# Kernel tuning notes

Hardware: AMD Instinct MI355X
Metric: run time of the kernel (lower is better)

The kernel has to match this reference:

```python
import jax, jax.numpy as jnp
from jax import lax
import numpy as np

NUM_CAPS = 4
CAP_DIM = 8
NUM_CLASSES = 10
CLASS_DIM = 16


def squash(x):
    # x: [..., D]; scale = |x|^2/(1+|x|^2)/sqrt(|x|^2+1e-8)
    sq = jnp.sum(x * x, axis=-1, keepdims=True)
    return sq / (1.0 + sq) / jnp.sqrt(sq + 1e-8) * x


def primary_caps(x, w, b):
    # x: [B,C,H,W], w: [32,C,3,3] -> caps [B, H*W*NUM_CAPS, CAP_DIM]
    out = lax.conv_general_dilated(
        x, w, window_strides=(1, 1), padding=[(1, 1), (1, 1)],
        dimension_numbers=('NCHW', 'OIHW', 'NCHW')) + b[None, :, None, None]
    B, C, H, W = out.shape
    out = out.reshape(B, NUM_CAPS, CAP_DIM, H * W)
    out = out.transpose(0, 3, 1, 2).reshape(B, H * W * NUM_CAPS, CAP_DIM)
    return squash(out)


def setup_inputs() -> dict:
    key = jax.random.key(0)
    ks = jax.random.split(key, 7)
    B, H, Wd = 64, 32, 32
    hsi_c, sar_c = 144, 4
    N = 2 * H * Wd * NUM_CAPS  # 8192
    return {
        'x_hsi': jax.random.normal(ks[0], (B, hsi_c, H, Wd), jnp.float32),
        'x_sar': jax.random.normal(ks[1], (B, sar_c, H, Wd), jnp.float32),
        'wh': jax.random.normal(ks[2], (NUM_CAPS * CAP_DIM, hsi_c, 3, 3), jnp.float32) * 0.05,
        'bh': jax.random.normal(ks[3], (NUM_CAPS * CAP_DIM,), jnp.float32) * 0.05,
        'ws': jax.random.normal(ks[4], (NUM_CAPS * CAP_DIM, sar_c, 3, 3), jnp.float32) * 0.05,
        'bs': jax.random.normal(ks[5], (NUM_CAPS * CAP_DIM,), jnp.float32) * 0.05,
        'W': jax.random.normal(ks[6], (N, NUM_CLASSES, CLASS_DIM, CAP_DIM), jnp.float32),
    }


def reference(x_hsi, x_sar, wh, bh, ws, bs, W):
    caps_h = primary_caps(x_hsi, wh, bh)
    caps_s = primary_caps(x_sar, ws, bs)
    caps = jnp.concatenate([caps_h, caps_s], axis=1)  # [B, N, D]
    N = caps.shape[1]
    # routing_iters=1 with b=0 => c = 1/N uniform; s = sum_n c*u_hat = mean_n u_hat
    # u_hat[b,n,c,j] = sum_d W[n,c,j,d] * caps[b,n,d] (fused, never materialized)
    s = jnp.einsum('bnd,ncjd->bcj', caps, W) / N  # [B, num_classes, class_dim]
    v = squash(s)
    logits = jnp.sqrt(jnp.sum(v * v, axis=-1))  # [B, num_classes]
    return logits
```

## Files before the change

### kernel.cpp

```cpp
#include <hip/hip_runtime.h>
#include <hip/hip_bf16.h>


#define B_SZ 64
#define HW 32

typedef __attribute__((ext_vector_type(8))) short bf16x8s;
typedef __attribute__((ext_vector_type(4))) float f32x4;

__device__ inline short f2bf(float f) {
    __hip_bfloat16 h = __float2bfloat16(f);
    return *reinterpret_cast<short*>(&h);
}

__global__ __launch_bounds__(256) void prep_w_kernel(const float* __restrict__ wh,
                                                     short* __restrict__ wtb) {
    int idx = blockIdx.x * 256 + threadIdx.x;
    int tap = idx / 5120;
    int rest = idx - tap * 5120;
    int oc = rest / 160;
    int cin = rest - oc * 160;
    short v = 0;
    if (cin < 144) v = f2bf(wh[(oc * 144 + cin) * 9 + tap]);
    wtb[idx] = v;
}

__global__ __launch_bounds__(256) void prep_x_kernel(const float* __restrict__ xin,
                                                     short* __restrict__ xb) {
    __shared__ short tile[160 * 33];
    int t = threadIdx.x;
    int b = blockIdx.x >> 5;
    int y = blockIdx.x & 31;
    for (int idx = t; idx < 512; idx += 256) {
        int x = idx & 31, cin = 144 + (idx >> 5);
        tile[cin * 33 + x] = 0;
    }
    for (int base = 0; base < 144; base += 8) {
        int cin = base + (t >> 5), x = t & 31;
        float v = xin[(((size_t)b * 144 + cin) * 32 + y) * 32 + x];
        tile[cin * 33 + x] = f2bf(v);
    }
    __syncthreads();
    unsigned* dst = (unsigned*)(xb + ((size_t)(b * 32 + y) * 32) * 160);
    for (int idx = t; idx < 2560; idx += 256) {
        int x = idx / 80;
        int cinp = idx - x * 80;
        unsigned lo = (unsigned short)tile[(2 * cinp) * 33 + x];
        unsigned hi = (unsigned short)tile[(2 * cinp + 1) * 33 + x];
        dst[idx] = lo | (hi << 16);
    }
}

__global__ void transpose_w_kernel(const float* __restrict__ w, float* __restrict__ wt,
                                   int cin_total) {
    int idx = blockIdx.x * blockDim.x + threadIdx.x;
    int total = 32 * cin_total * 9;
    if (idx >= total) return;
    int oc = idx & 31;
    int rest = idx >> 5;
    int tap = rest % 9;
    int cin = rest / 9;
    wt[idx] = w[(oc * cin_total + cin) * 9 + tap];
}

__global__ __launch_bounds__(256) void conv_mfma_kernel(
        const short* __restrict__ xb, const short* __restrict__ wtb,
        const float* __restrict__ bias, short* __restrict__ capsb) {
    __shared__ float ctile[64][34];
    int t = threadIdx.x;
    int l = t & 63;
    int wv = t >> 6;
    int mhalf = wv >> 1;
    int nt = wv & 1;
    int l15 = l & 15, lhi = l >> 4;
    int b = blockIdx.x >> 4;
    int y0 = (blockIdx.x & 15) << 1;
    int y = y0 + mhalf;
    int kofs = lhi * 8;

    const short* xbb = xb + (size_t)b * 1024 * 160;

    f32x4 acc0 = {0.f, 0.f, 0.f, 0.f};
    f32x4 acc1 = {0.f, 0.f, 0.f, 0.f};
    const bf16x8s zfrag = {0, 0, 0, 0, 0, 0, 0, 0};

    #pragma unroll
    for (int tap = 0; tap < 9; ++tap) {
        int dy = tap / 3, dx = tap % 3;
        int iy = y + dy - 1;
        bool rowok = (unsigned)iy < 32u;
        int iyc = rowok ? iy : 0;
        int ix0 = l15 + dx - 1;
        int ix1 = 16 + l15 + dx - 1;
        bool ok0 = rowok && ((unsigned)ix0 < 32u);
        bool ok1 = rowok && ((unsigned)ix1 < 32u);
        int ix0c = min(max(ix0, 0), 31);
        int ix1c = min(max(ix1, 0), 31);
        const short* xa0 = xbb + ((size_t)(iyc * 32 + ix0c)) * 160 + kofs;
        const short* xa1 = xbb + ((size_t)(iyc * 32 + ix1c)) * 160 + kofs;
        const short* wa = wtb + ((size_t)tap * 32 + nt * 16 + l15) * 160 + kofs;
        #pragma unroll
        for (int kc = 0; kc < 5; ++kc) {
            bf16x8s bfrag = *(const bf16x8s*)(wa + kc * 32);
            bf16x8s a0 = *(const bf16x8s*)(xa0 + kc * 32);
            bf16x8s a1 = *(const bf16x8s*)(xa1 + kc * 32);
            a0 = ok0 ? a0 : zfrag;
            a1 = ok1 ? a1 : zfrag;
            acc0 = __builtin_amdgcn_mfma_f32_16x16x32_bf16(a0, bfrag, acc0, 0, 0, 0);
            acc1 = __builtin_amdgcn_mfma_f32_16x16x32_bf16(a1, bfrag, acc1, 0, 0, 0);
        }
    }

    #pragma unroll
    for (int r = 0; r < 4; ++r) {
        ctile[mhalf * 32 + lhi * 4 + r][nt * 16 + l15] = acc0[r];
        ctile[mhalf * 32 + 16 + lhi * 4 + r][nt * 16 + l15] = acc1[r];
    }
    __syncthreads();

    int p = t >> 2;
    int cap = t & 3;
    float s[8];
    float sq = 0.0f;
    #pragma unroll
    for (int d = 0; d < 8; ++d) {
        s[d] = ctile[p][cap * 8 + d] + bias[cap * 8 + d];
        sq += s[d] * s[d];
    }
    float scale = sq / ((1.0f + sq) * sqrtf(sq + 1e-8f));
    int pix = (y0 + (p >> 5)) * 32 + (p & 31);
    int n = pix * 4 + cap;
    bf16x8s o;
    #pragma unroll
    for (int d = 0; d < 8; ++d) o[d] = f2bf(s[d] * scale);
    *(bf16x8s*)(capsb + ((size_t)b * 8192 + n) * 8) = o;
}

__global__ __launch_bounds__(256) void conv_caps_sar_kernel(
        const float* __restrict__ xin, const float* __restrict__ wt,
        const float* __restrict__ bias, short* __restrict__ capsb, int n_base) {
    constexpr int CIN = 4;
    __shared__ float red[4][32][64];
    int t = threadIdx.x;
    int wave = __builtin_amdgcn_readfirstlane(t >> 6);
    int lane = t & 63;
    int x = lane & 31;
    int yy = lane >> 5;
    int bidx = blockIdx.x;
    int b = bidx >> 4;
    int y = ((bidx & 15) << 1) + yy;

    const float* xb_ = xin + (size_t)b * CIN * (HW * HW);

    float acc[32];
    #pragma unroll
    for (int oc = 0; oc < 32; ++oc) acc[oc] = 0.0f;

    {
        int cin = wave;
        const float* xc = xb_ + (size_t)cin * (HW * HW);
        const float* wc = wt + (size_t)cin * 288;
        #pragma unroll
        for (int ky = 0; ky < 3; ++ky) {
            int iy = y + ky - 1;
            bool rowok = (iy >= 0) && (iy < HW);
            const float* xrow = xc + iy * HW;
            float v0 = (rowok && x > 0)      ? xrow[x - 1] : 0.0f;
            float v1 = rowok                 ? xrow[x]     : 0.0f;
            float v2 = (rowok && x < HW - 1) ? xrow[x + 1] : 0.0f;
            const float* wk = wc + ky * 96;
            #pragma unroll
            for (int oc = 0; oc < 32; ++oc) {
                acc[oc] += v0 * wk[oc] + v1 * wk[32 + oc] + v2 * wk[64 + oc];
            }
        }
    }

    #pragma unroll
    for (int oc = 0; oc < 32; ++oc) red[wave][oc][lane] = acc[oc];
    __syncthreads();

    int cap = t >> 6;
    int p = t & 63;
    float s[8];
    float sq = 0.0f;
    #pragma unroll
    for (int d = 0; d < 8; ++d) {
        int oc = cap * 8 + d;
        s[d] = bias[oc] + red[0][oc][p] + red[1][oc][p] + red[2][oc][p] + red[3][oc][p];
        sq += s[d] * s[d];
    }
    float scale = sq / ((1.0f + sq) * sqrtf(sq + 1e-8f));
    int pix = (((bidx & 15) << 1) + (p >> 5)) * HW + (p & 31);
    int n = n_base + pix * 4 + cap;
    bf16x8s o;
    #pragma unroll
    for (int d = 0; d < 8; ++d) o[d] = f2bf(s[d] * scale);
    *(bf16x8s*)(capsb + ((size_t)b * 8192 + n) * 8) = o;
}

__global__ __launch_bounds__(256) void routing_mfma_kernel(
        const short* __restrict__ capsb, const float* __restrict__ W,
        float* __restrict__ partials) {
    __shared__ float red[4][64][18];
    int t = threadIdx.x;
    int l = t & 63;
    int wv = t >> 6;
    int l15 = l & 15, lhi = l >> 4;
    int kc = blockIdx.x;
    int ntile = blockIdx.y;
    int cj = ntile * 16 + l15;

    f32x4 acc[4] = {{0.f,0.f,0.f,0.f},{0.f,0.f,0.f,0.f},{0.f,0.f,0.f,0.f},{0.f,0.f,0.f,0.f}};

    int kk0 = kc * 32 + wv * 8;
    for (int ks = 0; ks < 8; ++ks) {
        int n = (kk0 + ks) * 4 + lhi;
        const float* wp = W + ((size_t)n * 160 + cj) * 8;
        float4 w0 = *(const float4*)wp;
        float4 w1 = *(const float4*)(wp + 4);
        union { short s[8]; bf16x8s v; } bu;
        bu.s[0] = f2bf(w0.x); bu.s[1] = f2bf(w0.y);
        bu.s[2] = f2bf(w0.z); bu.s[3] = f2bf(w0.w);
        bu.s[4] = f2bf(w1.x); bu.s[5] = f2bf(w1.y);
        bu.s[6] = f2bf(w1.z); bu.s[7] = f2bf(w1.w);
        const short* ap = capsb + (size_t)n * 8;
        #pragma unroll
        for (int mt = 0; mt < 4; ++mt) {
            int b = mt * 16 + l15;
            bf16x8s afrag = *(const bf16x8s*)(ap + (size_t)b * 8192 * 8);
            acc[mt] = __builtin_amdgcn_mfma_f32_16x16x32_bf16(afrag, bu.v, acc[mt], 0, 0, 0);
        }
    }

    #pragma unroll
    for (int mt = 0; mt < 4; ++mt) {
        #pragma unroll
        for (int r = 0; r < 4; ++r) {
            red[wv][mt * 16 + lhi * 4 + r][l15] = acc[mt][r];
        }
    }
    __syncthreads();

    for (int idx = t; idx < 1024; idx += 256) {
        int b = idx >> 4, cjl = idx & 15;
        float sum = red[0][b][cjl] + red[1][b][cjl] + red[2][b][cjl] + red[3][b][cjl];
        partials[(((size_t)kc * 10 + ntile) * 64 + b) * 16 + cjl] = sum;
    }
}

__global__ __launch_bounds__(256) void finalize_kernel(
        const float* __restrict__ partials, float* __restrict__ out) {
    __shared__ float s_sh[160];
    int t = threadIdx.x;
    int b = blockIdx.x;
    if (t < 160) {
        int nt = t >> 4, cjl = t & 15;
        float s = 0.0f;
        #pragma unroll 8
        for (int kc = 0; kc < 64; ++kc)
            s += partials[(((size_t)kc * 10 + nt) * 64 + b) * 16 + cjl];
        s_sh[t] = s * (1.0f / 8192.0f);
    }
    __syncthreads();
    if (t < 10) {
        float sq = 0.0f;
        #pragma unroll
        for (int j = 0; j < 16; ++j) {
            float v = s_sh[t * 16 + j];
            sq += v * v;
        }
        float scale = sq / ((1.0f + sq) * sqrtf(sq + 1e-8f));
        out[b * 10 + t] = sqrtf(sq) * scale;
    }
}

extern "C" void kernel_launch(void* const* d_in, const int* in_sizes, int n_in,
                              void* d_out, int out_size, void* d_ws, size_t ws_size,
                              hipStream_t stream) {
    const float* x_hsi = (const float*)d_in[0];
    const float* x_sar = (const float*)d_in[1];
    const float* wh    = (const float*)d_in[2];
    const float* bh    = (const float*)d_in[3];
    const float* wsar  = (const float*)d_in[4];
    const float* bs    = (const float*)d_in[5];
    const float* W     = (const float*)d_in[6];
    float* out = (float*)d_out;

    char* ws = (char*)d_ws;
    short* wtb     = (short*)(ws + 0);
    float* wt_s    = (float*)(ws + 92672);
    short* xb      = (short*)(ws + 102400);
    short* capsb   = (short*)(ws + 21073920);
    float* partials = (float*)(ws + 29462528);

    prep_w_kernel<<<180, 256, 0, stream>>>(wh, wtb);
    prep_x_kernel<<<2048, 256, 0, stream>>>(x_hsi, xb);
    transpose_w_kernel<<<5, 256, 0, stream>>>(wsar, wt_s, 4);

    conv_mfma_kernel<<<1024, 256, 0, stream>>>(xb, wtb, bh, capsb);
    conv_caps_sar_kernel<<<1024, 256, 0, stream>>>(x_sar, wt_s, bs, capsb, 4096);

    routing_mfma_kernel<<<dim3(64, 10), 256, 0, stream>>>(capsb, W, partials);

    finalize_kernel<<<64, 256, 0, stream>>>(partials, out);
}
```

Baseline: 84.16 us.

## Fuse input conversion and both convolutions into one kernel, transpose caps layout

Drops the separate bf16 input-conversion and SAR weight transpose kernels. A single conv kernel now stages fp32 HSI rows into shared memory as bf16, computing four output rows per block with 2x2 MFMA tiles, while extra blocks compute the SAR conv directly. The caps buffer layout changes to [n][batch][8] so the routing kernel reads contiguous fragments, and routing uses twice as many K-split blocks. The intent is to remove the 20MB intermediate bf16 tensor round-trip and launch overhead. The SAR path is one block per image with serial scalar work, which may leave a long tail.

```diff
diff --git a/kernel.cpp b/kernel.cpp
--- a/kernel.cpp
+++ b/kernel.cpp
@@ -1,9 +1,6 @@
 #include <hip/hip_runtime.h>
 #include <hip/hip_bf16.h>
 
-
-#define B_SZ 64
-#define HW 32
 
 typedef __attribute__((ext_vector_type(8))) short bf16x8s;
 typedef __attribute__((ext_vector_type(4))) float f32x4;
@@ -16,6 +13,7 @@
 __global__ __launch_bounds__(256) void prep_w_kernel(const float* __restrict__ wh,
                                                      short* __restrict__ wtb) {
     int idx = blockIdx.x * 256 + threadIdx.x;
+    if (idx >= 46080) return;
     int tap = idx / 5120;
     int rest = idx - tap * 5120;
     int oc = rest / 160;
@@ -25,178 +23,155 @@
     wtb[idx] = v;
 }
 
-__global__ __launch_bounds__(256) void prep_x_kernel(const float* __restrict__ xin,
-                                                     short* __restrict__ xb) {
-    __shared__ short tile[160 * 33];
+__global__ __launch_bounds__(256) void conv_both_kernel(
+        const float* __restrict__ x_hsi, const short* __restrict__ wtb,
+        const float* __restrict__ bh,
+        const float* __restrict__ x_sar, const float* __restrict__ wsar,
+        const float* __restrict__ bs,
+        short* __restrict__ capsb) {
+    __shared__ union {
+        short xs[6][32][168];
+        float ct[128][33];
+    } sm;
     int t = threadIdx.x;
-    int b = blockIdx.x >> 5;
-    int y = blockIdx.x & 31;
-    for (int idx = t; idx < 512; idx += 256) {
-        int x = idx & 31, cin = 144 + (idx >> 5);
-        tile[cin * 33 + x] = 0;
-    }
-    for (int base = 0; base < 144; base += 8) {
-        int cin = base + (t >> 5), x = t & 31;
-        float v = xin[(((size_t)b * 144 + cin) * 32 + y) * 32 + x];
-        tile[cin * 33 + x] = f2bf(v);
-    }
-    __syncthreads();
-    unsigned* dst = (unsigned*)(xb + ((size_t)(b * 32 + y) * 32) * 160);
-    for (int idx = t; idx < 2560; idx += 256) {
-        int x = idx / 80;
-        int cinp = idx - x * 80;
-        unsigned lo = (unsigned short)tile[(2 * cinp) * 33 + x];
-        unsigned hi = (unsigned short)tile[(2 * cinp + 1) * 33 + x];
-        dst[idx] = lo | (hi << 16);
-    }
-}
-
-__global__ void transpose_w_kernel(const float* __restrict__ w, float* __restrict__ wt,
-                                   int cin_total) {
-    int idx = blockIdx.x * blockDim.x + threadIdx.x;
-    int total = 32 * cin_total * 9;
-    if (idx >= total) return;
-    int oc = idx & 31;
-    int rest = idx >> 5;
-    int tap = rest % 9;
-    int cin = rest / 9;
-    wt[idx] = w[(oc * cin_total + cin) * 9 + tap];
-}
-
-__global__ __launch_bounds__(256) void conv_mfma_kernel(
-        const short* __restrict__ xb, const short* __restrict__ wtb,
-        const float* __restrict__ bias, short* __restrict__ capsb) {
-    __shared__ float ctile[64][34];
-    int t = threadIdx.x;
-    int l = t & 63;
-    int wv = t >> 6;
-    int mhalf = wv >> 1;
-    int nt = wv & 1;
-    int l15 = l & 15, lhi = l >> 4;
-    int b = blockIdx.x >> 4;
-    int y0 = (blockIdx.x & 15) << 1;
-    int y = y0 + mhalf;
-    int kofs = lhi * 8;
-
-    const short* xbb = xb + (size_t)b * 1024 * 160;
-
-    f32x4 acc0 = {0.f, 0.f, 0.f, 0.f};
-    f32x4 acc1 = {0.f, 0.f, 0.f, 0.f};
-    const bf16x8s zfrag = {0, 0, 0, 0, 0, 0, 0, 0};
-
-    #pragma unroll
-    for (int tap = 0; tap < 9; ++tap) {
-        int dy = tap / 3, dx = tap % 3;
-        int iy = y + dy - 1;
-        bool rowok = (unsigned)iy < 32u;
-        int iyc = rowok ? iy : 0;
-        int ix0 = l15 + dx - 1;
-        int ix1 = 16 + l15 + dx - 1;
-        bool ok0 = rowok && ((unsigned)ix0 < 32u);
-        bool ok1 = rowok && ((unsigned)ix1 < 32u);
-        int ix0c = min(max(ix0, 0), 31);
-        int ix1c = min(max(ix1, 0), 31);
-        const short* xa0 = xbb + ((size_t)(iyc * 32 + ix0c)) * 160 + kofs;
-        const short* xa1 = xbb + ((size_t)(iyc * 32 + ix1c)) * 160 + kofs;
-        const short* wa = wtb + ((size_t)tap * 32 + nt * 16 + l15) * 160 + kofs;
-        #pragma unroll
-        for (int kc = 0; kc < 5; ++kc) {
-            bf16x8s bfrag = *(const bf16x8s*)(wa + kc * 32);
-            bf16x8s a0 = *(const bf16x8s*)(xa0 + kc * 32);
-            bf16x8s a1 = *(const bf16x8s*)(xa1 + kc * 32);
-            a0 = ok0 ? a0 : zfrag;
-            a1 = ok1 ? a1 : zfrag;
-            acc0 = __builtin_amdgcn_mfma_f32_16x16x32_bf16(a0, bfrag, acc0, 0, 0, 0);
-            acc1 = __builtin_amdgcn_mfma_f32_16x16x32_bf16(a1, bfrag, acc1, 0, 0, 0);
-        }
-    }
-
-    #pragma unroll
-    for (int r = 0; r < 4; ++r) {
-        ctile[mhalf * 32 + lhi * 4 + r][nt * 16 + l15] = acc0[r];
-        ctile[mhalf * 32 + 16 + lhi * 4 + r][nt * 16 + l15] = acc1[r];
-    }
-    __syncthreads();
-
-    int p = t >> 2;
-    int cap = t & 3;
-    float s[8];
-    float sq = 0.0f;
-    #pragma unroll
-    for (int d = 0; d < 8; ++d) {
-        s[d] = ctile[p][cap * 8 + d] + bias[cap * 8 + d];
-        sq += s[d] * s[d];
-    }
-    float scale = sq / ((1.0f + sq) * sqrtf(sq + 1e-8f));
-    int pix = (y0 + (p >> 5)) * 32 + (p & 31);
-    int n = pix * 4 + cap;
-    bf16x8s o;
-    #pragma unroll
-    for (int d = 0; d < 8; ++d) o[d] = f2bf(s[d] * scale);
-    *(bf16x8s*)(capsb + ((size_t)b * 8192 + n) * 8) = o;
-}
-
-__global__ __launch_bounds__(256) void conv_caps_sar_kernel(
-        const float* __restrict__ xin, const float* __restrict__ wt,
-        const float* __restrict__ bias, short* __restrict__ capsb, int n_base) {
-    constexpr int CIN = 4;
-    __shared__ float red[4][32][64];
-    int t = threadIdx.x;
-    int wave = __builtin_amdgcn_readfirstlane(t >> 6);
-    int lane = t & 63;
-    int x = lane & 31;
-    int yy = lane >> 5;
-    int bidx = blockIdx.x;
-    int b = bidx >> 4;
-    int y = ((bidx & 15) << 1) + yy;
-
-    const float* xb_ = xin + (size_t)b * CIN * (HW * HW);
-
-    float acc[32];
-    #pragma unroll
-    for (int oc = 0; oc < 32; ++oc) acc[oc] = 0.0f;
-
-    {
-        int cin = wave;
-        const float* xc = xb_ + (size_t)cin * (HW * HW);
-        const float* wc = wt + (size_t)cin * 288;
-        #pragma unroll
-        for (int ky = 0; ky < 3; ++ky) {
-            int iy = y + ky - 1;
-            bool rowok = (iy >= 0) && (iy < HW);
-            const float* xrow = xc + iy * HW;
-            float v0 = (rowok && x > 0)      ? xrow[x - 1] : 0.0f;
-            float v1 = rowok                 ? xrow[x]     : 0.0f;
-            float v2 = (rowok && x < HW - 1) ? xrow[x + 1] : 0.0f;
-            const float* wk = wc + ky * 96;
-            #pragma unroll
-            for (int oc = 0; oc < 32; ++oc) {
-                acc[oc] += v0 * wk[oc] + v1 * wk[32 + oc] + v2 * wk[64 + oc];
-            }
-        }
-    }
-
-    #pragma unroll
-    for (int oc = 0; oc < 32; ++oc) red[wave][oc][lane] = acc[oc];
-    __syncthreads();
-
-    int cap = t >> 6;
-    int p = t & 63;
-    float s[8];
-    float sq = 0.0f;
-    #pragma unroll
-    for (int d = 0; d < 8; ++d) {
-        int oc = cap * 8 + d;
-        s[d] = bias[oc] + red[0][oc][p] + red[1][oc][p] + red[2][oc][p] + red[3][oc][p];
-        sq += s[d] * s[d];
-    }
-    float scale = sq / ((1.0f + sq) * sqrtf(sq + 1e-8f));
-    int pix = (((bidx & 15) << 1) + (p >> 5)) * HW + (p & 31);
-    int n = n_base + pix * 4 + cap;
-    bf16x8s o;
-    #pragma unroll
-    for (int d = 0; d < 8; ++d) o[d] = f2bf(s[d] * scale);
-    *(bf16x8s*)(capsb + ((size_t)b * 8192 + n) * 8) = o;
+
+    if (blockIdx.x < 512) {
+        int b = blockIdx.x >> 3;
+        int y0 = (blockIdx.x & 7) << 2;
+
+        {
+            int x = t & 31;
+            int i0 = t >> 5;
+            const float* xb_ = x_hsi + (size_t)b * 144 * 1024;
+            for (int item = i0; item < 432; item += 8) {
+                int row = item / 72;
+                int cp = item - row * 72;
+                int iy = y0 - 1 + row;
+                unsigned u = 0;
+                if ((unsigned)iy < 32u) {
+                    float f0 = xb_[(size_t)(2 * cp) * 1024 + iy * 32 + x];
+                    float f1 = xb_[(size_t)(2 * cp + 1) * 1024 + iy * 32 + x];
+                    u = (unsigned)(unsigned short)f2bf(f0)
+                      | ((unsigned)(unsigned short)f2bf(f1) << 16);
+                }
+                *(unsigned*)&sm.xs[row][x][2 * cp] = u;
+            }
+            for (int item = i0; item < 48; item += 8) {
+                int row = item >> 3;
+                int c4 = item & 7;
+                *(unsigned*)&sm.xs[row][x][144 + 2 * c4] = 0;
+            }
+        }
+        __syncthreads();
+
+        int l = t & 63;
+        int wv = t >> 6;
+        int l15 = l & 15, lhi = l >> 4;
+        int kofs = lhi * 8;
+
+        f32x4 acc[2][2] = {{{0.f,0.f,0.f,0.f},{0.f,0.f,0.f,0.f}},
+                           {{0.f,0.f,0.f,0.f},{0.f,0.f,0.f,0.f}}};
+        const bf16x8s zf = {0,0,0,0,0,0,0,0};
+
+        #pragma unroll
+        for (int tap = 0; tap < 9; ++tap) {
+            int dy = tap / 3, dx = tap % 3;
+            int lrow = wv + dy;
+            int ix0 = l15 + dx - 1;
+            int ix1 = 16 + l15 + dx - 1;
+            bool ok0 = (unsigned)ix0 < 32u;
+            bool ok1 = (unsigned)ix1 < 32u;
+            int ix0c = ok0 ? ix0 : 0;
+            int ix1c = ok1 ? ix1 : 0;
+            const short* xa0 = &sm.xs[lrow][ix0c][kofs];
+            const short* xa1 = &sm.xs[lrow][ix1c][kofs];
+            const short* wa = wtb + ((size_t)tap * 32 + l15) * 160 + kofs;
+            #pragma unroll
+            for (int kc = 0; kc < 5; ++kc) {
+                bf16x8s a0 = *(const bf16x8s*)(xa0 + kc * 32);
+                bf16x8s a1 = *(const bf16x8s*)(xa1 + kc * 32);
+                a0 = ok0 ? a0 : zf;
+                a1 = ok1 ? a1 : zf;
+                bf16x8s b0 = *(const bf16x8s*)(wa + kc * 32);
+                bf16x8s b1 = *(const bf16x8s*)(wa + 16 * 160 + kc * 32);
+                acc[0][0] = __builtin_amdgcn_mfma_f32_16x16x32_bf16(a0, b0, acc[0][0], 0, 0, 0);
+                acc[0][1] = __builtin_amdgcn_mfma_f32_16x16x32_bf16(a0, b1, acc[0][1], 0, 0, 0);
+                acc[1][0] = __builtin_amdgcn_mfma_f32_16x16x32_bf16(a1, b0, acc[1][0], 0, 0, 0);
+                acc[1][1] = __builtin_amdgcn_mfma_f32_16x16x32_bf16(a1, b1, acc[1][1], 0, 0, 0);
+            }
+        }
+        __syncthreads();
+
+        #pragma unroll
+        for (int xh = 0; xh < 2; ++xh)
+            #pragma unroll
+            for (int nt = 0; nt < 2; ++nt)
+                #pragma unroll
+                for (int r = 0; r < 4; ++r)
+                    sm.ct[wv * 32 + xh * 16 + lhi * 4 + r][nt * 16 + l15] = acc[xh][nt][r];
+        __syncthreads();
+
+        #pragma unroll
+        for (int h = 0; h < 2; ++h) {
+            int q = t + h * 256;
+            int p = q >> 2;
+            int cap = q & 3;
+            float s[8];
+            float sq = 0.0f;
+            #pragma unroll
+            for (int d = 0; d < 8; ++d) {
+                s[d] = sm.ct[p][cap * 8 + d] + bh[cap * 8 + d];
+                sq += s[d] * s[d];
+            }
+            float scale = sq / ((1.0f + sq) * sqrtf(sq + 1e-8f));
+            int pix = (y0 + (p >> 5)) * 32 + (p & 31);
+            int n = pix * 4 + cap;
+            bf16x8s o;
+            #pragma unroll
+            for (int d = 0; d < 8; ++d) o[d] = f2bf(s[d] * scale);
+            *(bf16x8s*)(capsb + ((size_t)n * 64 + b) * 8) = o;
+        }
+    } else {
+        int b = blockIdx.x - 512;
+        const float* xb_ = x_sar + (size_t)b * 4 * 1024;
+        for (int i = 0; i < 4; ++i) {
+            int px = t + i * 256;
+            int y = px >> 5, x = px & 31;
+            float acc[32];
+            #pragma unroll
+            for (int oc = 0; oc < 32; ++oc) acc[oc] = bs[oc];
+            #pragma unroll
+            for (int tap = 0; tap < 9; ++tap) {
+                int dy = tap / 3, dx = tap % 3;
+                int iy = y + dy - 1, ix = x + dx - 1;
+                bool ok = ((unsigned)iy < 32u) && ((unsigned)ix < 32u);
+                int off = ok ? (iy * 32 + ix) : 0;
+                float v[4];
+                #pragma unroll
+                for (int ch = 0; ch < 4; ++ch) {
+                    float ld = xb_[(size_t)ch * 1024 + off];
+                    v[ch] = ok ? ld : 0.0f;
+                }
+                #pragma unroll
+                for (int oc = 0; oc < 32; ++oc)
+                    #pragma unroll
+                    for (int ch = 0; ch < 4; ++ch)
+                        acc[oc] += v[ch] * wsar[(oc * 4 + ch) * 9 + tap];
+            }
+            #pragma unroll
+            for (int cap = 0; cap < 4; ++cap) {
+                float sq = 0.0f;
+                #pragma unroll
+                for (int d = 0; d < 8; ++d) sq += acc[cap * 8 + d] * acc[cap * 8 + d];
+                float scale = sq / ((1.0f + sq) * sqrtf(sq + 1e-8f));
+                int n = 4096 + px * 4 + cap;
+                bf16x8s o;
+                #pragma unroll
+                for (int d = 0; d < 8; ++d) o[d] = f2bf(acc[cap * 8 + d] * scale);
+                *(bf16x8s*)(capsb + ((size_t)n * 64 + b) * 8) = o;
+            }
+        }
+    }
 }
 
 __global__ __launch_bounds__(256) void routing_mfma_kernel(
@@ -213,8 +188,9 @@
 
     f32x4 acc[4] = {{0.f,0.f,0.f,0.f},{0.f,0.f,0.f,0.f},{0.f,0.f,0.f,0.f},{0.f,0.f,0.f,0.f}};
 
-    int kk0 = kc * 32 + wv * 8;
-    for (int ks = 0; ks < 8; ++ks) {
+    int kk0 = kc * 16 + wv * 4;
+    #pragma unroll
+    for (int ks = 0; ks < 4; ++ks) {
         int n = (kk0 + ks) * 4 + lhi;
         const float* wp = W + ((size_t)n * 160 + cj) * 8;
         float4 w0 = *(const float4*)wp;
@@ -224,22 +200,19 @@
         bu.s[2] = f2bf(w0.z); bu.s[3] = f2bf(w0.w);
         bu.s[4] = f2bf(w1.x); bu.s[5] = f2bf(w1.y);
         bu.s[6] = f2bf(w1.z); bu.s[7] = f2bf(w1.w);
-        const short* ap = capsb + (size_t)n * 8;
+        const short* ap = capsb + (size_t)n * 512;
         #pragma unroll
         for (int mt = 0; mt < 4; ++mt) {
-            int b = mt * 16 + l15;
-            bf16x8s afrag = *(const bf16x8s*)(ap + (size_t)b * 8192 * 8);
+            bf16x8s afrag = *(const bf16x8s*)(ap + (mt * 16 + l15) * 8);
             acc[mt] = __builtin_amdgcn_mfma_f32_16x16x32_bf16(afrag, bu.v, acc[mt], 0, 0, 0);
         }
     }
 
     #pragma unroll
-    for (int mt = 0; mt < 4; ++mt) {
-        #pragma unroll
-        for (int r = 0; r < 4; ++r) {
+    for (int mt = 0; mt < 4; ++mt)
+        #pragma unroll
+        for (int r = 0; r < 4; ++r)
             red[wv][mt * 16 + lhi * 4 + r][l15] = acc[mt][r];
-        }
-    }
     __syncthreads();
 
     for (int idx = t; idx < 1024; idx += 256) {
@@ -258,7 +231,7 @@
         int nt = t >> 4, cjl = t & 15;
         float s = 0.0f;
         #pragma unroll 8
-        for (int kc = 0; kc < 64; ++kc)
+        for (int kc = 0; kc < 128; ++kc)
             s += partials[(((size_t)kc * 10 + nt) * 64 + b) * 16 + cjl];
         s_sh[t] = s * (1.0f / 8192.0f);
     }
@@ -288,20 +261,15 @@
     float* out = (float*)d_out;
 
     char* ws = (char*)d_ws;
-    short* wtb     = (short*)(ws + 0);
-    float* wt_s    = (float*)(ws + 92672);
-    short* xb      = (short*)(ws + 102400);
-    short* capsb   = (short*)(ws + 21073920);
-    float* partials = (float*)(ws + 29462528);
+    short* wtb      = (short*)(ws + 0);
+    short* capsb    = (short*)(ws + 131072);
+    float* partials = (float*)(ws + 8519680);
 
     prep_w_kernel<<<180, 256, 0, stream>>>(wh, wtb);
-    prep_x_kernel<<<2048, 256, 0, stream>>>(x_hsi, xb);
-    transpose_w_kernel<<<5, 256, 0, stream>>>(wsar, wt_s, 4);
-
-    conv_mfma_kernel<<<1024, 256, 0, stream>>>(xb, wtb, bh, capsb);
-    conv_caps_sar_kernel<<<1024, 256, 0, stream>>>(x_sar, wt_s, bs, capsb, 4096);
-
-    routing_mfma_kernel<<<dim3(64, 10), 256, 0, stream>>>(capsb, W, partials);
+
+    conv_both_kernel<<<576, 256, 0, stream>>>(x_hsi, wtb, bh, x_sar, wsar, bs, capsb);
+
+    routing_mfma_kernel<<<dim3(128, 10), 256, 0, stream>>>(capsb, W, partials);
 
     finalize_kernel<<<64, 256, 0, stream>>>(partials, out);
 }
```

Measured after the change: 142.6 us. 69.5% more time.
